# Kernel tuning notes

Hardware: AMD Instinct MI355X
Metric: run time of the kernel (lower is better)

The kernel has to match this reference:

```python
import jax, jax.numpy as jnp
import numpy as np

HIDDEN = 1024
HEADS = 16
HEAD_DIM = HIDDEN // HEADS


def setup_inputs() -> dict:
    key = jax.random.key(0)
    ks = jax.random.split(key, 5)
    x = jax.random.normal(ks[0], (4, 2048, HIDDEN), dtype=jnp.float32)
    s = 1.0 / np.sqrt(HIDDEN)
    W_qkv = jax.random.normal(ks[1], (HIDDEN, 3 * HIDDEN), dtype=jnp.float32) * s
    b_qkv = jax.random.normal(ks[2], (3 * HIDDEN,), dtype=jnp.float32) * s
    W_out = jax.random.normal(ks[3], (HIDDEN, HIDDEN), dtype=jnp.float32) * s
    b_out = jax.random.normal(ks[4], (HIDDEN,), dtype=jnp.float32) * s
    return {"x": x, "W_qkv": W_qkv, "b_qkv": b_qkv, "W_out": W_out, "b_out": b_out}


def reference(x, W_qkv, b_qkv, W_out, b_out):
    B, S, _ = x.shape
    qkv = x @ W_qkv + b_qkv                       # [B,S,3H]
    qkv = qkv.reshape(B, S, 3, HEADS, HEAD_DIM)
    q, k, v = jnp.moveaxis(qkv, 2, 0)             # each [B,S,nh,hd]
    scale = 1.0 / np.sqrt(HEAD_DIM)
    scores = jnp.einsum('bqhd,bkhd->bhqk', q, k) * scale
    probs = jax.nn.softmax(scores, axis=-1)       # dropout p=0 (eval): identity
    attn = jnp.einsum('bhqk,bkhd->bqhd', probs, v)
    attn = attn.reshape(B, S, HIDDEN)
    return attn @ W_out + b_out
```

## Files before the change

kernel.cpp:

```cpp
#include <hip/hip_runtime.h>

#define SEQ    2048
#define BATCH  4
#define HID    1024
#define NH     16
#define MTOT   (BATCH * SEQ)

typedef __attribute__((ext_vector_type(8)))  short          short8;
typedef __attribute__((ext_vector_type(4)))  float          f32x4;
typedef __attribute__((ext_vector_type(16))) float          f32x16;
typedef __attribute__((ext_vector_type(8)))  unsigned short ushort8v;
typedef __attribute__((ext_vector_type(4)))  unsigned int   uint4v;

#define QSCL 0.125f

__device__ __forceinline__ float bf2f(unsigned short u) {
    return __uint_as_float(((unsigned int)u) << 16);
}
__device__ __forceinline__ unsigned short f2bf(float f) {
    unsigned int u = __float_as_uint(f);
    u += 0x7fffu + ((u >> 16) & 1u);
    return (unsigned short)(u >> 16);
}
__device__ __forceinline__ unsigned int pk2bf(float lo, float hi) {
    unsigned int ul = __float_as_uint(lo) + 0x8000u;
    unsigned int uh = __float_as_uint(hi) + 0x8000u;
    return __builtin_amdgcn_perm(uh, ul, 0x07060302u);
}

__device__ __forceinline__ void gl_lds16(const void* g, void* l) {
    __builtin_amdgcn_global_load_lds(
        (__attribute__((address_space(1))) void*)g,
        (__attribute__((address_space(3))) void*)l, 16, 0, 0);
}

__device__ __forceinline__ int swz64(int row, int col) {
    return row * 64 + ((((col >> 3) ^ (row & 7))) << 3) + (col & 7);
}

__device__ __forceinline__ int gidx64(int row, int kq) {
    return (row * 8 + ((kq + (row & 7)) & 7)) * 8;
}

__global__ __launch_bounds__(256)
void cvt_x(const float* __restrict__ x, unsigned short* __restrict__ xb)
{
    const size_t i = ((size_t)blockIdx.x * 256 + threadIdx.x) * 4;
    const float4 f = *(const float4*)(x + i);
    uint2 u;
    u.x = pk2bf(f.x, f.y);
    u.y = pk2bf(f.z, f.w);
    *(uint2*)(xb + i) = u;
}

__global__ __launch_bounds__(256)
void transpose_cvt(const float* __restrict__ W, unsigned short* __restrict__ Wt,
                   int K, int N)
{
    __shared__ unsigned short T[32][33];
    const int n0 = blockIdx.x * 32, k0 = blockIdx.y * 32;
    const int tr = threadIdx.x >> 3, tc = (threadIdx.x & 7) * 4;
    const float4 f = *(const float4*)(W + (size_t)(k0 + tr) * N + n0 + tc);
    T[tr][tc + 0] = f2bf(f.x);
    T[tr][tc + 1] = f2bf(f.y);
    T[tr][tc + 2] = f2bf(f.z);
    T[tr][tc + 3] = f2bf(f.w);
    __syncthreads();
    ushort4 u;
    u.x = T[tc + 0][tr]; u.y = T[tc + 1][tr];
    u.z = T[tc + 2][tr]; u.w = T[tc + 3][tr];
    *(ushort4*)(Wt + (size_t)(n0 + tr) * K + k0 + tc) = u;
}

template<bool OUTF32, bool VSPLIT, bool BIASROW>
__global__ __launch_bounds__(256)
void gemm_mfma(const unsigned short* __restrict__ A,
               const unsigned short* __restrict__ Bt,
               const float* __restrict__ bias, void* __restrict__ Cptr,
               int lda, int ldc, int K)
{
    __shared__ unsigned short As[128 * 64];
    __shared__ unsigned short Bs[128 * 64];

    const int tid = threadIdx.x;
    const int wave = tid >> 6, lane = tid & 63;
    const int quad = lane >> 4, lm = lane & 15;
    const int wm = wave & 1, wn = wave >> 1;
    const int m0 = blockIdx.y * 128, n0 = blockIdx.x * 128;

    const unsigned short* aSrc[4];
    const unsigned short* bSrc[4];
    unsigned short* aDst[4];
    unsigned short* bDst[4];
    #pragma unroll
    for (int j = 0; j < 4; ++j) {
        const int g = (wave * 4 + j) * 64 + lane;
        const int row = g >> 3;
        const int kq = ((g & 7) - (row & 7)) & 7;
        aSrc[j] = A  + (size_t)(m0 + row) * lda + kq * 8;
        bSrc[j] = Bt + (size_t)(n0 + row) * K   + kq * 8;
        aDst[j] = &As[g * 8];
        bDst[j] = &Bs[g * 8];
    }

    f32x4 acc[4][4];
    #pragma unroll
    for (int i = 0; i < 4; ++i)
        #pragma unroll
        for (int j = 0; j < 4; ++j)
            acc[i][j] = (f32x4){0.f, 0.f, 0.f, 0.f};

    int aOff[2][4], bOff[2][4];
    #pragma unroll
    for (int h = 0; h < 2; ++h)
        #pragma unroll
        for (int i = 0; i < 4; ++i) {
            aOff[h][i] = gidx64(wm * 64 + i * 16 + lm, h * 4 + quad);
            bOff[h][i] = gidx64(wn * 64 + i * 16 + lm, h * 4 + quad);
        }

    for (int k0 = 0; k0 < K; k0 += 64) {
        __syncthreads();
        #pragma unroll
        for (int j = 0; j < 4; ++j) gl_lds16(aSrc[j] + k0, aDst[j]);
        #pragma unroll
        for (int j = 0; j < 4; ++j) gl_lds16(bSrc[j] + k0, bDst[j]);
        __syncthreads();

        #pragma unroll
        for (int h = 0; h < 2; ++h) {
            short8 af[4], bf[4];
            #pragma unroll
            for (int i = 0; i < 4; ++i) af[i] = *(const short8*)&As[aOff[h][i]];
            #pragma unroll
            for (int j = 0; j < 4; ++j) bf[j] = *(const short8*)&Bs[bOff[h][j]];
            #pragma unroll
            for (int i = 0; i < 4; ++i)
                #pragma unroll
                for (int j = 0; j < 4; ++j)
                    acc[i][j] = __builtin_amdgcn_mfma_f32_16x16x32_bf16(
                        af[i], bf[j], acc[i][j], 0, 0, 0);
        }
    }

    float bj[4];
    float br[4][4];
    if constexpr (BIASROW) {
        #pragma unroll
        for (int i = 0; i < 4; ++i) {
            const float4 t =
                *(const float4*)(bias + m0 + wm * 64 + i * 16 + quad * 4);
            br[i][0] = t.x; br[i][1] = t.y; br[i][2] = t.z; br[i][3] = t.w;
        }
    } else {
        #pragma unroll
        for (int j = 0; j < 4; ++j) bj[j] = bias[n0 + wn * 64 + j * 16 + lm];
    }

    #pragma unroll
    for (int i = 0; i < 4; ++i) {
        #pragma unroll
        for (int j = 0; j < 4; ++j) {
            const int col = n0 + wn * 64 + j * 16 + lm;
            #pragma unroll
            for (int rr = 0; rr < 4; ++rr) {
                const int row = m0 + wm * 64 + i * 16 + quad * 4 + rr;
                float v = acc[i][j][rr] + (BIASROW ? br[i][rr] : bj[j]);
                if constexpr (VSPLIT) {
                    if (col < 1024) v *= QSCL;
                    ((unsigned short*)Cptr)[(size_t)row * ldc + col] = f2bf(v);
                } else if constexpr (OUTF32) {
                    ((float*)Cptr)[(size_t)row * ldc + col] = v;
                } else {
                    ((unsigned short*)Cptr)[(size_t)row * ldc + col] = f2bf(v);
                }
            }
        }
    }
}

__global__ __launch_bounds__(256, 2)
void attn_mfma(unsigned short* __restrict__ qk,
               const unsigned short* __restrict__ Vt)
{
    const int qt = blockIdx.x, hh = blockIdx.y, b = blockIdx.z;
    const size_t row0 = (size_t)b * SEQ;
    const int tid = threadIdx.x;
    const int wave = tid >> 6, lane = tid & 63;
    const int l5 = lane >> 5, lm = lane & 31;

    __shared__ unsigned short Ks[2][64 * 64];
    __shared__ unsigned short Vs[2][64 * 64];

    const int qbase = qt * 256 + wave * 64;

    short8 qf[2][4];
    #pragma unroll
    for (int qg = 0; qg < 2; ++qg)
        #pragma unroll
        for (int ks = 0; ks < 4; ++ks)
            qf[qg][ks] = *(const short8*)(
                qk + (row0 + qbase + qg * 32 + lm) * 2048 + hh * 64 + ks * 16 + l5 * 8);

    f32x16 oacc[2][2];
    #pragma unroll
    for (int dg = 0; dg < 2; ++dg)
        #pragma unroll
        for (int qg = 0; qg < 2; ++qg)
            #pragma unroll
            for (int e = 0; e < 16; ++e) oacc[dg][qg][e] = 0.f;
    float lrun[2] = {0.f, 0.f};

    const unsigned short* kSrc[2];
    const unsigned short* vSrc[2];
    int dOff[2];
    #pragma unroll
    for (int jj = 0; jj < 2; ++jj) {
        const int g = (wave * 2 + jj) * 64 + lane;
        const int row = g >> 3, slot = g & 7;
        const int colg = slot ^ (row & 7);
        kSrc[jj] = qk + 1024 + hh * 64 + (row0 + row) * 2048 + colg * 8;
        vSrc[jj] = Vt + (size_t)(hh * 64 + row) * (size_t)MTOT
                      + (size_t)b * SEQ + colg * 8;
        dOff[jj] = g * 8;
    }

    #pragma unroll
    for (int jj = 0; jj < 2; ++jj) {
        gl_lds16(kSrc[jj], &Ks[0][dOff[jj]]);
        gl_lds16(vSrc[jj], &Vs[0][dOff[jj]]);
    }
    __syncthreads();

    int cur = 0;
    for (int kt = 0; kt < SEQ; kt += 64) {
        if (kt + 64 < SEQ) {
            const size_t ko = (size_t)(kt + 64) * 2048;
            const int vo = kt + 64;
            #pragma unroll
            for (int jj = 0; jj < 2; ++jj) {
                gl_lds16(kSrc[jj] + ko, &Ks[cur ^ 1][dOff[jj]]);
                gl_lds16(vSrc[jj] + vo, &Vs[cur ^ 1][dOff[jj]]);
            }
        }
        const unsigned short* ksc = Ks[cur];
        const unsigned short* vsc = Vs[cur];

        #pragma unroll
        for (int kg = 0; kg < 2; ++kg) {
            short8 aK[4];
            #pragma unroll
            for (int ks = 0; ks < 4; ++ks)
                aK[ks] = *(const short8*)&ksc[swz64(kg * 32 + lm, ks * 16 + l5 * 8)];

            f32x16 s[2];
            #pragma unroll
            for (int qg = 0; qg < 2; ++qg) {
                #pragma unroll
                for (int e = 0; e < 16; ++e) s[qg][e] = 0.f;
                __builtin_amdgcn_s_setprio(1);
                #pragma unroll
                for (int ks = 0; ks < 4; ++ks)
                    s[qg] = __builtin_amdgcn_mfma_f32_32x32x16_bf16(
                        aK[ks], qf[qg][ks], s[qg], 0, 0, 0);
                __builtin_amdgcn_s_setprio(0);
                float ls = 0.f;
                #pragma unroll
                for (int rg = 0; rg < 4; ++rg) {
                    const float p0 = __expf(s[qg][rg * 4 + 0]);
                    const float p1 = __expf(s[qg][rg * 4 + 1]);
                    const float p2 = __expf(s[qg][rg * 4 + 2]);
                    const float p3 = __expf(s[qg][rg * 4 + 3]);
                    s[qg][rg * 4 + 0] = p0; s[qg][rg * 4 + 1] = p1;
                    s[qg][rg * 4 + 2] = p2; s[qg][rg * 4 + 3] = p3;
                    ls += (p0 + p1) + (p2 + p3);
                }
                lrun[qg] += ls;
            }

            #pragma unroll
            for (int step = 0; step < 2; ++step) {
                const int ks = kg * 2 + step;
                const short8 aV0 =
                    *(const short8*)&vsc[swz64(lm,      ks * 16 + l5 * 8)];
                const short8 aV1 =
                    *(const short8*)&vsc[swz64(32 + lm, ks * 16 + l5 * 8)];
                #pragma unroll
                for (int qg = 0; qg < 2; ++qg) {
                    const int b0 = step * 8;
                    const unsigned int u  = pk2bf(s[qg][b0 + 0], s[qg][b0 + 1]);
                    const unsigned int vv = pk2bf(s[qg][b0 + 2], s[qg][b0 + 3]);
                    const unsigned int u2 = pk2bf(s[qg][b0 + 4], s[qg][b0 + 5]);
                    const unsigned int v2 = pk2bf(s[qg][b0 + 6], s[qg][b0 + 7]);
                    const auto rA =
                        __builtin_amdgcn_permlane32_swap(u,  u2, false, false);
                    const auto rB =
                        __builtin_amdgcn_permlane32_swap(vv, v2, false, false);
                    uint4v wv;
                    wv.x = rA[0]; wv.y = rB[0]; wv.z = rA[1]; wv.w = rB[1];
                    const short8 bP = __builtin_bit_cast(short8, wv);
                    __builtin_amdgcn_s_setprio(1);
                    oacc[0][qg] = __builtin_amdgcn_mfma_f32_32x32x16_bf16(
                        aV0, bP, oacc[0][qg], 0, 0, 0);
                    oacc[1][qg] = __builtin_amdgcn_mfma_f32_32x32x16_bf16(
                        aV1, bP, oacc[1][qg], 0, 0, 0);
                    __builtin_amdgcn_s_setprio(0);
                }
            }
        }
        __syncthreads();
        cur ^= 1;
    }

    float linv[2];
    #pragma unroll
    for (int qg = 0; qg < 2; ++qg) {
        const float lt = lrun[qg] + __shfl_xor(lrun[qg], 32);
        linv[qg] = 1.f / lt;
    }

    #pragma unroll
    for (int dg = 0; dg < 2; ++dg)
        #pragma unroll
        for (int qg = 0; qg < 2; ++qg) {
            unsigned short* orow =
                qk + (row0 + qbase + qg * 32 + lm) * 2048 + hh * 64;
            #pragma unroll
            for (int rg = 0; rg < 4; ++rg) {
                const int d0 = dg * 32 + rg * 8 + l5 * 4;
                ushort4 st;
                st.x = f2bf(oacc[dg][qg][rg * 4 + 0] * linv[qg]);
                st.y = f2bf(oacc[dg][qg][rg * 4 + 1] * linv[qg]);
                st.z = f2bf(oacc[dg][qg][rg * 4 + 2] * linv[qg]);
                st.w = f2bf(oacc[dg][qg][rg * 4 + 3] * linv[qg]);
                *(ushort4*)(orow + d0) = st;
            }
        }
}

__global__ __launch_bounds__(256)
void qproj(const float* __restrict__ A, const float* __restrict__ W,
           const float* __restrict__ bias, unsigned short* __restrict__ outus)
{
    __shared__ float As[64][17];
    __shared__ float Bs[16][64];
    const int tid = threadIdx.x;
    const int tx = tid & 15, ty = tid >> 4;
    const int m0 = blockIdx.y * 64, n0 = blockIdx.x * 64;
    const int ar = tid >> 2, ac = (tid & 3) * 4;
    const int br = tid >> 4, bc = (tid & 15) * 4;
    float acc[4][4] = {{0.f}};
    for (int k0 = 0; k0 < HID; k0 += 16) {
        const float4 av = *(const float4*)(A + (size_t)(m0 + ar) * HID + k0 + ac);
        As[ar][ac + 0] = av.x; As[ar][ac + 1] = av.y;
        As[ar][ac + 2] = av.z; As[ar][ac + 3] = av.w;
        *(float4*)&Bs[br][bc] =
            *(const float4*)(W + (size_t)(k0 + br) * 3072 + n0 + bc);
        __syncthreads();
        #pragma unroll
        for (int kk = 0; kk < 16; ++kk) {
            float a[4];
            #pragma unroll
            for (int i = 0; i < 4; ++i) a[i] = As[ty * 4 + i][kk];
            const float4 b4 = *(const float4*)&Bs[kk][tx * 4];
            const float bv[4] = {b4.x, b4.y, b4.z, b4.w};
            #pragma unroll
            for (int i = 0; i < 4; ++i)
                #pragma unroll
                for (int j = 0; j < 4; ++j)
                    acc[i][j] = fmaf(a[i], bv[j], acc[i][j]);
        }
        __syncthreads();
    }
    float bb[4];
    #pragma unroll
    for (int j = 0; j < 4; ++j) bb[j] = bias[n0 + tx * 4 + j];
    #pragma unroll
    for (int i = 0; i < 4; ++i) {
        ushort4 st;
        st.x = f2bf(acc[i][0] + bb[0]); st.y = f2bf(acc[i][1] + bb[1]);
        st.z = f2bf(acc[i][2] + bb[2]); st.w = f2bf(acc[i][3] + bb[3]);
        *(ushort4*)(outus + (size_t)(m0 + ty * 4 + i) * 2048 + 1024 + n0 + tx * 4) = st;
    }
}

__global__ __launch_bounds__(256)
void kv_inplace(const float* __restrict__ W, const float* __restrict__ bias,
                unsigned short* __restrict__ xu)
{
    const float* xf = (const float*)xu;
    __shared__ unsigned short Asb[16][1032];
    __shared__ float Bs[16][68];
    const int tid = threadIdx.x;
    const int m0 = blockIdx.x * 16;
    const int tx = tid & 15, ty = tid >> 4;
    #pragma unroll 4
    for (int i = 0; i < 16; ++i) {
        const float4 v = *(const float4*)(xf + (size_t)(m0 + i) * HID + tid * 4);
        ushort4 s;
        s.x = f2bf(v.x); s.y = f2bf(v.y); s.z = f2bf(v.z); s.w = f2bf(v.w);
        *(ushort4*)&Asb[i][tid * 4] = s;
    }
    __syncthreads();
    for (int n0 = 0; n0 < 2048; n0 += 64) {
        float acc[4] = {0.f, 0.f, 0.f, 0.f};
        for (int k0 = 0; k0 < HID; k0 += 16) {
            *(float4*)&Bs[ty][tx * 4] =
                *(const float4*)(W + (size_t)(k0 + ty) * 3072 + 1024 + n0 + tx * 4);
            __syncthreads();
            #pragma unroll
            for (int kk = 0; kk < 16; ++kk) {
                const float a = bf2f(Asb[ty][k0 + kk]);
                const float4 b4 = *(const float4*)&Bs[kk][tx * 4];
                acc[0] = fmaf(a, b4.x, acc[0]); acc[1] = fmaf(a, b4.y, acc[1]);
                acc[2] = fmaf(a, b4.z, acc[2]); acc[3] = fmaf(a, b4.w, acc[3]);
            }
            __syncthreads();
        }
        const int n = n0 + tx * 4;
        ushort4 s;
        s.x = f2bf(acc[0] + bias[1024 + n + 0]);
        s.y = f2bf(acc[1] + bias[1024 + n + 1]);
        s.z = f2bf(acc[2] + bias[1024 + n + 2]);
        s.w = f2bf(acc[3] + bias[1024 + n + 3]);
        *(ushort4*)(xu + (size_t)(m0 + ty) * 2048 + n) = s;
    }
}

__global__ __launch_bounds__(256)
void attn_fwd(const unsigned short* __restrict__ xu,
              unsigned short* __restrict__ outus)
{
    const int qt = blockIdx.x, h = blockIdx.y, b = blockIdx.z;
    const int s0 = qt * 16;
    const size_t row0 = (size_t)b * SEQ;
    const int tid = threadIdx.x;
    const int qi = tid >> 4, tj = tid & 15;
    __shared__ float Ksh[64][68];
    __shared__ float Vsh[64][68];
    __shared__ float Psh[16][68];
    float qreg[64];
    {
        const uint4* qp =
            (const uint4*)(outus + (row0 + s0 + qi) * 2048 + 1024 + h * 64);
        #pragma unroll
        for (int i = 0; i < 8; ++i) {
            uint4 u = qp[i];
            const unsigned int w[4] = {u.x, u.y, u.z, u.w};
            #pragma unroll
            for (int j = 0; j < 4; ++j) {
                qreg[i * 8 + j * 2 + 0] = __uint_as_float(w[j] << 16) * 0.125f;
                qreg[i * 8 + j * 2 + 1] = __uint_as_float(w[j] & 0xffff0000u) * 0.125f;
            }
        }
    }
    float mrun = -1e30f, lrunv = 0.f;
    float oacc[4] = {0.f, 0.f, 0.f, 0.f};
    const int lr = tid >> 3, lc = (tid & 7) * 8;
    for (int kt = 0; kt < SEQ; kt += 64) {
        __syncthreads();
        #pragma unroll
        for (int half = 0; half < 2; ++half) {
            const int r = lr + half * 32;
            const size_t rowoff = (row0 + kt + r) * 2048 + h * 64 + lc;
            uint4 ku = *(const uint4*)(xu + rowoff);
            uint4 vu = *(const uint4*)(xu + rowoff + 1024);
            float4 f0, f1;
            f0.x = __uint_as_float(ku.x << 16); f0.y = __uint_as_float(ku.x & 0xffff0000u);
            f0.z = __uint_as_float(ku.y << 16); f0.w = __uint_as_float(ku.y & 0xffff0000u);
            f1.x = __uint_as_float(ku.z << 16); f1.y = __uint_as_float(ku.z & 0xffff0000u);
            f1.z = __uint_as_float(ku.w << 16); f1.w = __uint_as_float(ku.w & 0xffff0000u);
            *(float4*)&Ksh[r][lc]     = f0;
            *(float4*)&Ksh[r][lc + 4] = f1;
            f0.x = __uint_as_float(vu.x << 16); f0.y = __uint_as_float(vu.x & 0xffff0000u);
            f0.z = __uint_as_float(vu.y << 16); f0.w = __uint_as_float(vu.y & 0xffff0000u);
            f1.x = __uint_as_float(vu.z << 16); f1.y = __uint_as_float(vu.z & 0xffff0000u);
            f1.z = __uint_as_float(vu.w << 16); f1.w = __uint_as_float(vu.w & 0xffff0000u);
            *(float4*)&Vsh[r][lc]     = f0;
            *(float4*)&Vsh[r][lc + 4] = f1;
        }
        __syncthreads();
        float sc[4];
        #pragma unroll
        for (int u = 0; u < 4; ++u) {
            const int kk = tj + 16 * u;
            float s = 0.f;
            #pragma unroll
            for (int d = 0; d < 64; ++d) s = fmaf(qreg[d], Ksh[kk][d], s);
            sc[u] = s;
        }
        float tmax = fmaxf(fmaxf(sc[0], sc[1]), fmaxf(sc[2], sc[3]));
        #pragma unroll
        for (int off = 8; off >= 1; off >>= 1)
            tmax = fmaxf(tmax, __shfl_xor(tmax, off, 16));
        const float mnew = fmaxf(mrun, tmax);
        const float alpha = __expf(mrun - mnew);
        float psum = 0.f;
        #pragma unroll
        for (int u = 0; u < 4; ++u) {
            const float p = __expf(sc[u] - mnew);
            Psh[qi][tj + 16 * u] = p;
            psum += p;
        }
        #pragma unroll
        for (int off = 8; off >= 1; off >>= 1)
            psum += __shfl_xor(psum, off, 16);
        lrunv = lrunv * alpha + psum;
        mrun = mnew;
        oacc[0] *= alpha; oacc[1] *= alpha; oacc[2] *= alpha; oacc[3] *= alpha;
        __syncthreads();
        #pragma unroll 8
        for (int kk = 0; kk < 64; ++kk) {
            const float p = Psh[qi][kk];
            const float4 v4 = *(const float4*)&Vsh[kk][tj * 4];
            oacc[0] = fmaf(p, v4.x, oacc[0]); oacc[1] = fmaf(p, v4.y, oacc[1]);
            oacc[2] = fmaf(p, v4.z, oacc[2]); oacc[3] = fmaf(p, v4.w, oacc[3]);
        }
    }
    const float inv = 1.f / lrunv;
    ushort4 st;
    st.x = f2bf(oacc[0] * inv); st.y = f2bf(oacc[1] * inv);
    st.z = f2bf(oacc[2] * inv); st.w = f2bf(oacc[3] * inv);
    *(ushort4*)(outus + (row0 + s0 + qi) * 2048 + h * 64 + tj * 4) = st;
}

__global__ __launch_bounds__(256)
void out_final(const float* __restrict__ W, const float* __restrict__ bias,
               unsigned short* __restrict__ outus)
{
    float* outf = (float*)outus;
    __shared__ unsigned short Asb[16][1032];
    __shared__ float Bs[16][68];
    const int tid = threadIdx.x;
    const int m0 = blockIdx.x * 16;
    const int tx = tid & 15, ty = tid >> 4;
    #pragma unroll 4
    for (int i = 0; i < 16; ++i)
        *(ushort4*)&Asb[i][tid * 4] =
            *(const ushort4*)(outus + (size_t)(m0 + i) * 2048 + tid * 4);
    __syncthreads();
    for (int n0 = 0; n0 < 1024; n0 += 64) {
        float acc[4] = {0.f, 0.f, 0.f, 0.f};
        for (int k0 = 0; k0 < HID; k0 += 16) {
            *(float4*)&Bs[ty][tx * 4] =
                *(const float4*)(W + (size_t)(k0 + ty) * HID + n0 + tx * 4);
            __syncthreads();
            #pragma unroll
            for (int kk = 0; kk < 16; ++kk) {
                const float a = bf2f(Asb[ty][k0 + kk]);
                const float4 b4 = *(const float4*)&Bs[kk][tx * 4];
                acc[0] = fmaf(a, b4.x, acc[0]); acc[1] = fmaf(a, b4.y, acc[1]);
                acc[2] = fmaf(a, b4.z, acc[2]); acc[3] = fmaf(a, b4.w, acc[3]);
            }
            __syncthreads();
        }
        const int n = n0 + tx * 4;
        float4 st;
        st.x = acc[0] + bias[n + 0]; st.y = acc[1] + bias[n + 1];
        st.z = acc[2] + bias[n + 2]; st.w = acc[3] + bias[n + 3];
        *(float4*)(outf + (size_t)(m0 + ty) * HID + n) = st;
    }
}

extern "C" void kernel_launch(void* const* d_in, const int* in_sizes, int n_in,
                              void* d_out, int out_size, void* d_ws, size_t ws_size,
                              hipStream_t stream) {
    const float* x     = (const float*)d_in[0];
    const float* W_qkv = (const float*)d_in[1];
    const float* b_qkv = (const float*)d_in[2];
    const float* W_out = (const float*)d_in[3];
    const float* b_out = (const float*)d_in[4];

    dim3 blk(256);

    if (ws_size >= (size_t)56 * 1024 * 1024) {
        unsigned short* qkbuf  = (unsigned short*)d_ws;
        unsigned short* vtbuf  = qkbuf + (size_t)MTOT * 2048;
        unsigned short* wqkv_t = vtbuf + (size_t)1024 * MTOT;
        unsigned short* wout_t = wqkv_t + (size_t)3072 * 1024;
        unsigned short* xb     = (unsigned short*)d_out;

        cvt_x<<<dim3(MTOT * HID / 1024), blk, 0, stream>>>(x, xb);
        transpose_cvt<<<dim3(3072 / 32, 1024 / 32), blk, 0, stream>>>(
            W_qkv, wqkv_t, 1024, 3072);
        transpose_cvt<<<dim3(1024 / 32, 1024 / 32), blk, 0, stream>>>(
            W_out, wout_t, 1024, 1024);
        gemm_mfma<false, true, false><<<dim3(2048 / 128, MTOT / 128), blk, 0, stream>>>(
            xb, wqkv_t, b_qkv, (void*)qkbuf, 1024, 2048, 1024);
        gemm_mfma<false, false, true><<<dim3(MTOT / 128, 1024 / 128), blk, 0, stream>>>(
            wqkv_t + (size_t)2048 * 1024, xb, b_qkv + 2048, (void*)vtbuf,
            1024, MTOT, 1024);
        attn_mfma<<<dim3(SEQ / 256, NH, BATCH), blk, 0, stream>>>(qkbuf, vtbuf);
        gemm_mfma<true, false, false><<<dim3(1024 / 128, MTOT / 128), blk, 0, stream>>>(
            qkbuf, wout_t, b_out, d_out, 2048, 1024, 1024);
    } else {
        unsigned short* outus = (unsigned short*)d_out;
        unsigned short* xu    = (unsigned short*)d_in[0];
        qproj<<<dim3(HID / 64, MTOT / 64), blk, 0, stream>>>(x, W_qkv, b_qkv, outus);
        kv_inplace<<<dim3(MTOT / 16), blk, 0, stream>>>(W_qkv, b_qkv, xu);
        attn_fwd<<<dim3(SEQ / 16, NH, BATCH), blk, 0, stream>>>(xu, outus);
        out_final<<<dim3(MTOT / 16), blk, 0, stream>>>(W_out, b_out, outus);
    }
}
```

Measured before the change: 286.4 us.

## Split attention key range across two wave groups and merge partial outputs in LDS

The attention kernel now launches 512 threads per block: two groups of four waves each process half of the key sequence (split-K) for the same query tile, with both halves' K/V tiles double-buffered in shared memory. At the end, the second group writes its partial output accumulators and row sums to LDS (reusing the K/V buffer via a union), and the first group adds them before normalising and storing. The intent is to double the number of waves in flight per query tile to improve latency hiding and CU utilisation with only 512 blocks. The cost is more LDS, a final reduction pass with an extra barrier, and tighter register limits from the higher launch bound.

```diff
diff --git a/kernel.cpp b/kernel.cpp
--- a/kernel.cpp
+++ b/kernel.cpp
@@ -179,7 +179,7 @@
     }
 }
 
-__global__ __launch_bounds__(256, 2)
+__global__ __launch_bounds__(512, 4)
 void attn_mfma(unsigned short* __restrict__ qk,
                const unsigned short* __restrict__ Vt)
 {
@@ -187,12 +187,20 @@
     const size_t row0 = (size_t)b * SEQ;
     const int tid = threadIdx.x;
     const int wave = tid >> 6, lane = tid & 63;
+    const int wq = wave & 3;
+    const int kh = wave >> 2;
     const int l5 = lane >> 5, lm = lane & 31;
 
-    __shared__ unsigned short Ks[2][64 * 64];
-    __shared__ unsigned short Vs[2][64 * 64];
-
-    const int qbase = qt * 256 + wave * 64;
+    __shared__ union {
+        struct {
+            unsigned short Ks[2][2][64 * 64];
+            unsigned short Vs[2][2][64 * 64];
+        } t;
+        float Ocmb[4][64][64];
+    } u;
+    __shared__ float Lcmb[4][2][64];
+
+    const int qbase = qt * 256 + wq * 64;
 
     short8 qf[2][4];
     #pragma unroll
@@ -211,40 +219,39 @@
             for (int e = 0; e < 16; ++e) oacc[dg][qg][e] = 0.f;
     float lrun[2] = {0.f, 0.f};
 
-    const unsigned short* kSrc[2];
-    const unsigned short* vSrc[2];
-    int dOff[2];
-    #pragma unroll
-    for (int jj = 0; jj < 2; ++jj) {
-        const int g = (wave * 2 + jj) * 64 + lane;
-        const int row = g >> 3, slot = g & 7;
-        const int colg = slot ^ (row & 7);
-        kSrc[jj] = qk + 1024 + hh * 64 + (row0 + row) * 2048 + colg * 8;
-        vSrc[jj] = Vt + (size_t)(hh * 64 + row) * (size_t)MTOT
-                      + (size_t)b * SEQ + colg * 8;
-        dOff[jj] = g * 8;
-    }
-
-    #pragma unroll
-    for (int jj = 0; jj < 2; ++jj) {
-        gl_lds16(kSrc[jj], &Ks[0][dOff[jj]]);
-        gl_lds16(vSrc[jj], &Vs[0][dOff[jj]]);
+    const int g    = wave * 64 + lane;
+    const int grow = g >> 3, gslot = g & 7;
+    const int colg = gslot ^ (grow & 7);
+    const int dOff = g * 8;
+    const unsigned short* kSrcH[2];
+    const unsigned short* vSrcH[2];
+    #pragma unroll
+    for (int h = 0; h < 2; ++h) {
+        kSrcH[h] = qk + 1024 + hh * 64 + (row0 + h * 1024 + grow) * 2048 + colg * 8;
+        vSrcH[h] = Vt + (size_t)(hh * 64 + grow) * (size_t)MTOT
+                      + (size_t)b * SEQ + h * 1024 + colg * 8;
+    }
+
+    #pragma unroll
+    for (int h = 0; h < 2; ++h) {
+        gl_lds16(kSrcH[h], &u.t.Ks[0][h][dOff]);
+        gl_lds16(vSrcH[h], &u.t.Vs[0][h][dOff]);
     }
     __syncthreads();
 
     int cur = 0;
-    for (int kt = 0; kt < SEQ; kt += 64) {
-        if (kt + 64 < SEQ) {
-            const size_t ko = (size_t)(kt + 64) * 2048;
-            const int vo = kt + 64;
-            #pragma unroll
-            for (int jj = 0; jj < 2; ++jj) {
-                gl_lds16(kSrc[jj] + ko, &Ks[cur ^ 1][dOff[jj]]);
-                gl_lds16(vSrc[jj] + vo, &Vs[cur ^ 1][dOff[jj]]);
-            }
-        }
-        const unsigned short* ksc = Ks[cur];
-        const unsigned short* vsc = Vs[cur];
+    for (int st = 0; st < 16; ++st) {
+        if (st + 1 < 16) {
+            const size_t ko = (size_t)((st + 1) * 64) * 2048;
+            const int vo = (st + 1) * 64;
+            #pragma unroll
+            for (int h = 0; h < 2; ++h) {
+                gl_lds16(kSrcH[h] + ko, &u.t.Ks[cur ^ 1][h][dOff]);
+                gl_lds16(vSrcH[h] + vo, &u.t.Vs[cur ^ 1][h][dOff]);
+            }
+        }
+        const unsigned short* ksc = u.t.Ks[cur][kh];
+        const unsigned short* vsc = u.t.Vs[cur][kh];
 
         #pragma unroll
         for (int kg = 0; kg < 2; ++kg) {
@@ -288,12 +295,12 @@
                 #pragma unroll
                 for (int qg = 0; qg < 2; ++qg) {
                     const int b0 = step * 8;
-                    const unsigned int u  = pk2bf(s[qg][b0 + 0], s[qg][b0 + 1]);
+                    const unsigned int uu = pk2bf(s[qg][b0 + 0], s[qg][b0 + 1]);
                     const unsigned int vv = pk2bf(s[qg][b0 + 2], s[qg][b0 + 3]);
                     const unsigned int u2 = pk2bf(s[qg][b0 + 4], s[qg][b0 + 5]);
                     const unsigned int v2 = pk2bf(s[qg][b0 + 6], s[qg][b0 + 7]);
                     const auto rA =
-                        __builtin_amdgcn_permlane32_swap(u,  u2, false, false);
+                        __builtin_amdgcn_permlane32_swap(uu, u2, false, false);
                     const auto rB =
                         __builtin_amdgcn_permlane32_swap(vv, v2, false, false);
                     uint4v wv;
@@ -312,30 +319,54 @@
         cur ^= 1;
     }
 
-    float linv[2];
-    #pragma unroll
-    for (int qg = 0; qg < 2; ++qg) {
-        const float lt = lrun[qg] + __shfl_xor(lrun[qg], 32);
-        linv[qg] = 1.f / lt;
-    }
-
-    #pragma unroll
-    for (int dg = 0; dg < 2; ++dg)
+    if (kh == 1) {
+        #pragma unroll
+        for (int dg = 0; dg < 2; ++dg)
+            #pragma unroll
+            for (int qg = 0; qg < 2; ++qg)
+                #pragma unroll
+                for (int e = 0; e < 16; ++e)
+                    u.Ocmb[wq][(dg * 2 + qg) * 16 + e][lane] = oacc[dg][qg][e];
+        Lcmb[wq][0][lane] = lrun[0];
+        Lcmb[wq][1][lane] = lrun[1];
+    }
+    __syncthreads();
+    if (kh == 0) {
+        #pragma unroll
+        for (int dg = 0; dg < 2; ++dg)
+            #pragma unroll
+            for (int qg = 0; qg < 2; ++qg)
+                #pragma unroll
+                for (int e = 0; e < 16; ++e)
+                    oacc[dg][qg][e] += u.Ocmb[wq][(dg * 2 + qg) * 16 + e][lane];
+        lrun[0] += Lcmb[wq][0][lane];
+        lrun[1] += Lcmb[wq][1][lane];
+
+        float linv[2];
         #pragma unroll
         for (int qg = 0; qg < 2; ++qg) {
-            unsigned short* orow =
-                qk + (row0 + qbase + qg * 32 + lm) * 2048 + hh * 64;
-            #pragma unroll
-            for (int rg = 0; rg < 4; ++rg) {
-                const int d0 = dg * 32 + rg * 8 + l5 * 4;
-                ushort4 st;
-                st.x = f2bf(oacc[dg][qg][rg * 4 + 0] * linv[qg]);
-                st.y = f2bf(oacc[dg][qg][rg * 4 + 1] * linv[qg]);
-                st.z = f2bf(oacc[dg][qg][rg * 4 + 2] * linv[qg]);
-                st.w = f2bf(oacc[dg][qg][rg * 4 + 3] * linv[qg]);
-                *(ushort4*)(orow + d0) = st;
-            }
-        }
+            const float lt = lrun[qg] + __shfl_xor(lrun[qg], 32);
+            linv[qg] = 1.f / lt;
+        }
+
+        #pragma unroll
+        for (int dg = 0; dg < 2; ++dg)
+            #pragma unroll
+            for (int qg = 0; qg < 2; ++qg) {
+                unsigned short* orow =
+                    qk + (row0 + qbase + qg * 32 + lm) * 2048 + hh * 64;
+                #pragma unroll
+                for (int rg = 0; rg < 4; ++rg) {
+                    const int d0 = dg * 32 + rg * 8 + l5 * 4;
+                    ushort4 st;
+                    st.x = f2bf(oacc[dg][qg][rg * 4 + 0] * linv[qg]);
+                    st.y = f2bf(oacc[dg][qg][rg * 4 + 1] * linv[qg]);
+                    st.z = f2bf(oacc[dg][qg][rg * 4 + 2] * linv[qg]);
+                    st.w = f2bf(oacc[dg][qg][rg * 4 + 3] * linv[qg]);
+                    *(ushort4*)(orow + d0) = st;
+                }
+            }
+    }
 }
 
 __global__ __launch_bounds__(256)
@@ -590,7 +621,7 @@
         gemm_mfma<false, false, true><<<dim3(MTOT / 128, 1024 / 128), blk, 0, stream>>>(
             wqkv_t + (size_t)2048 * 1024, xb, b_qkv + 2048, (void*)vtbuf,
             1024, MTOT, 1024);
-        attn_mfma<<<dim3(SEQ / 256, NH, BATCH), blk, 0, stream>>>(qkbuf, vtbuf);
+        attn_mfma<<<dim3(SEQ / 256, NH, BATCH), dim3(512), 0, stream>>>(qkbuf, vtbuf);
         gemm_mfma<true, false, false><<<dim3(1024 / 128, MTOT / 128), blk, 0, stream>>>(
             qkbuf, wout_t, b_out, d_out, 2048, 1024, 1024);
     } else {
```

Measured after the change: 990.3 us. 3.46x slower.
